# Optimization experiments

Measured on AMD Instinct MI355X. Metric: run time of the kernel, lower is better.

The kernel has to match this reference:

```python
import jax, jax.numpy as jnp
import numpy as np

N = 100000      # nodes (single ntype)
R = 4           # edge types (relations)
E = 160000      # edges per relation
D_IN = 128
D_OUT = 128


def setup_inputs() -> dict:
    key = jax.random.key(0)
    k1, k2, k3, k4, k5 = jax.random.split(key, 5)
    gain = np.sqrt(2.0)  # calculate_gain('relu')
    bound = gain * np.sqrt(6.0 / (D_IN + D_OUT))  # xavier_uniform
    return {
        "x": jax.random.normal(k1, (N, D_IN), dtype=jnp.float32),
        "weight": jax.random.uniform(k2, (R, D_IN, D_OUT), dtype=jnp.float32,
                                     minval=-bound, maxval=bound),
        "loop_weight": jax.random.uniform(k3, (D_IN, D_OUT), dtype=jnp.float32,
                                          minval=-bound, maxval=bound),
        "h_bias": jnp.zeros((D_OUT,), dtype=jnp.float32),
        "src_idx": jax.random.randint(k4, (R, E), 0, N),
        "dst_idx": jax.random.randint(k5, (R, E), 0, N),
    }


def reference(x, weight, loop_weight, h_bias, src_idx, dst_idx):
    # Per-relation GraphConv(norm='right', weight external):
    #   h_r = segment_sum((x @ W_r)[src], dst) / clamp(in_degree, 1)
    # HeteroGraphConv default aggregation sums relations per dst node.
    n = x.shape[0]
    xw = jnp.einsum('nd,rdo->rno', x, weight)  # [R, N, D_OUT]
    h = jnp.zeros((n, weight.shape[2]), dtype=x.dtype)
    ones = jnp.ones((src_idx.shape[1],), dtype=x.dtype)
    for r in range(weight.shape[0]):  # small fixed relation count
        msg = xw[r][src_idx[r]]                                   # [E, D_OUT]
        agg = jax.ops.segment_sum(msg, dst_idx[r], num_segments=n)
        deg = jax.ops.segment_sum(ones, dst_idx[r], num_segments=n)
        h = h + agg / jnp.clip(deg, 1.0)[:, None]                 # norm='right'
    # self-loop + bias + activation (dropout=0 -> identity)
    h = h + x @ loop_weight + h_bias
    return jax.nn.relu(h)
```

## Files before the change

### kernel.cpp

```cpp
#include <hip/hip_runtime.h>

#define DD 128
#define KY 512
#define KT 640
#define RR 4
#define BKT 16
#define CAPS 15
#define NKS (KT / 32)

typedef short short8 __attribute__((ext_vector_type(8)));
typedef float f32x4 __attribute__((ext_vector_type(4)));

union U4S8 { uint4 u; short8 s; };

__device__ __forceinline__ unsigned short f2bf(float f) {
  unsigned u = __float_as_uint(f);
  u += 0x7fffu + ((u >> 16) & 1u);
  return (unsigned short)(u >> 16);
}

__global__ __launch_bounds__(256) void prep(const float* __restrict__ x,
                                            const float* __restrict__ weight,
                                            const float* __restrict__ loopw,
                                            const int* __restrict__ src,
                                            const int* __restrict__ dst,
                                            unsigned short* __restrict__ xb,
                                            unsigned short* __restrict__ wt,
                                            int* __restrict__ slot,
                                            int N, int E, int XB, int WB) {
  int b = blockIdx.x;
  int t = threadIdx.x;
  if (b < XB) {
    int i = b * 256 + t;
    if (i >= (N + 1) * 16) return;
    int n = i >> 4;
    uint4 o = make_uint4(0, 0, 0, 0);
    if (n < N) {
      const float4* xp = (const float4*)x + (size_t)i * 2;
      float4 v0 = xp[0], v1 = xp[1];
      o.x = (unsigned)f2bf(v0.x) | ((unsigned)f2bf(v0.y) << 16);
      o.y = (unsigned)f2bf(v0.z) | ((unsigned)f2bf(v0.w) << 16);
      o.z = (unsigned)f2bf(v1.x) | ((unsigned)f2bf(v1.y) << 16);
      o.w = (unsigned)f2bf(v1.z) | ((unsigned)f2bf(v1.w) << 16);
    }
    ((uint4*)xb)[i] = o;
  } else if (b < XB + WB) {
    int i = (b - XB) * 256 + t;
    if (i >= DD * KT) return;
    int j = i & 7, l = (i >> 3) & 63, c = (i >> 9) & 7, ks = i >> 12;
    int k = ks * 32 + (l >> 4) * 8 + j;
    int col = c * 16 + (l & 15);
    float v = (k < KY) ? weight[(size_t)((k >> 7) * DD + (k & (DD - 1))) * DD + col]
                       : loopw[(size_t)(k - KY) * DD + col];
    wt[i] = f2bf(v);
  } else {
    int i = (b - XB - WB) * 256 + t;
    if (i >= RR * E) return;
    int r = i / E;
    size_t base = ((size_t)dst[i] * RR + r) * BKT;
    int pos = atomicAdd(slot + base, 1);
    if (pos < CAPS) slot[base + 1 + pos] = src[i];
  }
}

__global__ __launch_bounds__(256) void gather_agg(const unsigned* __restrict__ xbu,
                                                  const int* __restrict__ slot,
                                                  unsigned* __restrict__ yu,
                                                  int NN ) {
  int gid = blockIdx.x * 256 + threadIdx.x;
  int n = gid >> 6, lane = gid & 63;
  if (n >= NN) return;
  int N = NN - 1;

  int sv = slot[(size_t)n * 64 + lane];

  int cn[RR], ct[RR];
#pragma unroll
  for (int r = 0; r < RR; r++) {
    ct[r] = __builtin_amdgcn_readlane(sv, r << 4);
    cn[r] = ct[r] > CAPS ? CAPS : ct[r];
  }

  float ax[RR], ay[RR];
#pragma unroll
  for (int r = 0; r < RR; r++) { ax[r] = 0.f; ay[r] = 0.f; }

  int m = max(max(cn[0], cn[1]), max(cn[2], cn[3]));
  for (int i0 = 0; i0 < m; i0 += 4) {
    unsigned vv[4][RR];
#pragma unroll
    for (int u = 0; u < 4; u++) {
#pragma unroll
      for (int r = 0; r < RR; r++) {
        int i = i0 + u;
        int ii = i > 14 ? 14 : i;
        int s = __builtin_amdgcn_readlane(sv, (r << 4) + 1 + ii);
        s = (i < cn[r]) ? s : N;
        vv[u][r] = xbu[(size_t)s * 64 + lane];
      }
    }
#pragma unroll
    for (int u = 0; u < 4; u++)
#pragma unroll
      for (int r = 0; r < RR; r++) {
        ax[r] += __uint_as_float(vv[u][r] << 16);
        ay[r] += __uint_as_float(vv[u][r] & 0xffff0000u);
      }
  }
#pragma unroll
  for (int r = 0; r < RR; r++) {
    float inv = 1.0f / (float)max(ct[r], 1);
    yu[(size_t)n * (KY / 2) + r * 64 + lane] =
        (unsigned)f2bf(ax[r] * inv) | ((unsigned)f2bf(ay[r] * inv) << 16);
  }
}

__global__ __launch_bounds__(512) void gemm_mfma(const unsigned short* __restrict__ y,
                                                 const unsigned short* __restrict__ xb,
                                                 const uint4* __restrict__ wtv,
                                                 const float* __restrict__ bias,
                                                 float* __restrict__ out, int N) {
  __shared__ __align__(16) unsigned short Bs[2][4096];
  int t = threadIdx.x;
  int w = t >> 6, lane = t & 63;
  int m = lane & 15, q = lane >> 4;
  int rb = blockIdx.x * 256;

  int grow0 = rb + w * 32 + m, grow1 = grow0 + 16;
  int r0c = grow0 > N ? N : grow0;
  int r1c = grow1 > N ? N : grow1;
  const unsigned short* ay0 = y  + (size_t)r0c * KY + q * 8;
  const unsigned short* ay1 = y  + (size_t)r1c * KY + q * 8;
  const unsigned short* ax0 = xb + (size_t)r0c * DD + q * 8;
  const unsigned short* ax1 = xb + (size_t)r1c * DD + q * 8;

  *(uint4*)(&Bs[0][t * 8]) = wtv[t];
  __syncthreads();

  f32x4 acc[2][8];
#pragma unroll
  for (int i = 0; i < 2; i++)
#pragma unroll
    for (int c = 0; c < 8; c++) acc[i][c] = (f32x4){0.f, 0.f, 0.f, 0.f};

#pragma unroll
  for (int ks = 0; ks < NKS; ++ks) {
    const int buf = ks & 1;
    uint4 bs;
    if (ks + 1 < NKS) bs = wtv[(size_t)(ks + 1) * 512 + t];

    U4S8 a0, a1;
    if (ks < 16) {
      a0.u = *(const uint4*)(ay0 + ks * 32);
      a1.u = *(const uint4*)(ay1 + ks * 32);
    } else {
      a0.u = *(const uint4*)(ax0 + (ks - 16) * 32);
      a1.u = *(const uint4*)(ax1 + (ks - 16) * 32);
    }

    short8 bb[8];
#pragma unroll
    for (int c = 0; c < 8; ++c)
      bb[c] = *(const short8*)(&Bs[buf][(c * 64 + lane) * 8]);

#pragma unroll
    for (int c = 0; c < 8; ++c) {
      acc[0][c] = __builtin_amdgcn_mfma_f32_16x16x32_bf16(a0.s, bb[c], acc[0][c], 0, 0, 0);
      acc[1][c] = __builtin_amdgcn_mfma_f32_16x16x32_bf16(a1.s, bb[c], acc[1][c], 0, 0, 0);
    }

    if (ks + 1 < NKS) {
      *(uint4*)(&Bs[buf ^ 1][t * 8]) = bs;
      __syncthreads();
    }
  }

  float bv[8];
#pragma unroll
  for (int c = 0; c < 8; ++c) bv[c] = bias[c * 16 + m];
#pragma unroll
  for (int i = 0; i < 2; ++i) {
    int rbase = rb + w * 32 + i * 16 + q * 4;
#pragma unroll
    for (int v = 0; v < 4; ++v) {
      int gr = rbase + v;
      if (gr < N) {
#pragma unroll
        for (int c = 0; c < 8; ++c)
          out[(size_t)gr * DD + c * 16 + m] = fmaxf(acc[i][c][v] + bv[c], 0.f);
      }
    }
  }
}

extern "C" void kernel_launch(void* const* d_in, const int* in_sizes, int n_in,
                              void* d_out, int out_size, void* d_ws, size_t ws_size,
                              hipStream_t stream) {
  const float* x      = (const float*)d_in[0];
  const float* weight = (const float*)d_in[1];
  const float* loop_w = (const float*)d_in[2];
  const float* h_bias = (const float*)d_in[3];
  const int*   src    = (const int*)d_in[4];
  const int*   dst    = (const int*)d_in[5];
  float* out = (float*)d_out;

  const int N = in_sizes[0] / DD;
  const int R = in_sizes[1] / (DD * DD);
  const int E = in_sizes[4] / R;
  const int RE = R * E;

  char* p = (char*)d_ws;
  auto alloc = [&](size_t bytes) {
    char* q = p;
    p += (bytes + 63) & ~size_t(63);
    return q;
  };
  int* slot = (int*)alloc((size_t)(N + 1) * RR * BKT * 4);
  unsigned short* wt = (unsigned short*)alloc((size_t)DD * KT * 2);
  unsigned short* xb = (unsigned short*)alloc((size_t)(N + 1) * DD * 2);
  unsigned short* y  = (unsigned short*)alloc((size_t)(N + 1) * KY * 2);

  hipMemsetAsync(slot, 0, (size_t)(N + 1) * RR * BKT * 4, stream);

  int XB = ((N + 1) * 16 + 255) / 256;
  int WB = (DD * KT + 255) / 256;
  int FB = (RE + 255) / 256;
  prep<<<XB + WB + FB, 256, 0, stream>>>(x, weight, loop_w, src, dst,
                                         xb, wt, slot, N, E, XB, WB);
  gather_agg<<<((size_t)(N + 1) * 64 + 255) / 256, 256, 0, stream>>>(
      (const unsigned*)xb, slot, (unsigned*)y, N + 1);
  gemm_mfma<<<(N + 255) / 256, 512, 0, stream>>>(y, xb, (const uint4*)wt,
                                                 h_bias, out, N);
}
```

Baseline: 230.1 us.

## Fuse neighbor gather-aggregation into the MFMA GEMM via shared-memory A tiles

Merges the gather/mean-aggregation kernel and the bf16 MFMA GEMM into one kernel. Each 256-thread block aggregates 64 nodes' per-relation means into a swizzled LDS tile and then multiplies that tile directly against the weight panels. This removes the intermediate y buffer (N x 512 bf16) write and re-read plus one kernel launch. It also switches the bf16 packing to the hardware v_cvt_pk_bf16_f32 instruction. In exchange it uses about 80KB of LDS per block, which limits occupancy, and each wave now does 16 rows of gather serially before its MFMA work.

```diff
diff --git a/kernel.cpp b/kernel.cpp
--- a/kernel.cpp
+++ b/kernel.cpp
@@ -17,6 +17,12 @@
   unsigned u = __float_as_uint(f);
   u += 0x7fffu + ((u >> 16) & 1u);
   return (unsigned short)(u >> 16);
+}
+
+__device__ __forceinline__ unsigned cvtpk(float lo, float hi) {
+  unsigned r;
+  asm("v_cvt_pk_bf16_f32 %0, %1, %2" : "=v"(r) : "v"(lo), "v"(hi));
+  return r;
 }
 
 __global__ __launch_bounds__(256) void prep(const float* __restrict__ x,
@@ -63,99 +69,112 @@
   }
 }
 
-__global__ __launch_bounds__(256) void gather_agg(const unsigned* __restrict__ xbu,
-                                                  const int* __restrict__ slot,
-                                                  unsigned* __restrict__ yu,
-                                                  int NN ) {
-  int gid = blockIdx.x * 256 + threadIdx.x;
-  int n = gid >> 6, lane = gid & 63;
-  if (n >= NN) return;
-  int N = NN - 1;
-
-  int sv = slot[(size_t)n * 64 + lane];
-
-  int cn[RR], ct[RR];
-#pragma unroll
-  for (int r = 0; r < RR; r++) {
-    ct[r] = __builtin_amdgcn_readlane(sv, r << 4);
-    cn[r] = ct[r] > CAPS ? CAPS : ct[r];
-  }
-
-  float ax[RR], ay[RR];
-#pragma unroll
-  for (int r = 0; r < RR; r++) { ax[r] = 0.f; ay[r] = 0.f; }
-
-  int m = max(max(cn[0], cn[1]), max(cn[2], cn[3]));
-  for (int i0 = 0; i0 < m; i0 += 4) {
-    unsigned vv[4][RR];
-#pragma unroll
-    for (int u = 0; u < 4; u++) {
-#pragma unroll
-      for (int r = 0; r < RR; r++) {
-        int i = i0 + u;
-        int ii = i > 14 ? 14 : i;
-        int s = __builtin_amdgcn_readlane(sv, (r << 4) + 1 + ii);
-        s = (i < cn[r]) ? s : N;
-        vv[u][r] = xbu[(size_t)s * 64 + lane];
-      }
-    }
-#pragma unroll
-    for (int u = 0; u < 4; u++)
-#pragma unroll
-      for (int r = 0; r < RR; r++) {
-        ax[r] += __uint_as_float(vv[u][r] << 16);
-        ay[r] += __uint_as_float(vv[u][r] & 0xffff0000u);
-      }
-  }
-#pragma unroll
-  for (int r = 0; r < RR; r++) {
-    float inv = 1.0f / (float)max(ct[r], 1);
-    yu[(size_t)n * (KY / 2) + r * 64 + lane] =
-        (unsigned)f2bf(ax[r] * inv) | ((unsigned)f2bf(ay[r] * inv) << 16);
-  }
-}
-
-__global__ __launch_bounds__(512) void gemm_mfma(const unsigned short* __restrict__ y,
-                                                 const unsigned short* __restrict__ xb,
-                                                 const uint4* __restrict__ wtv,
-                                                 const float* __restrict__ bias,
-                                                 float* __restrict__ out, int N) {
+__global__ __launch_bounds__(256) void gagemm(const unsigned* __restrict__ xbu,
+                                              const int* __restrict__ slotg,
+                                              const uint4* __restrict__ wtv,
+                                              const float* __restrict__ bias,
+                                              float* __restrict__ out, int N) {
+  __shared__ unsigned As[64 * 256];
   __shared__ __align__(16) unsigned short Bs[2][4096];
   int t = threadIdx.x;
   int w = t >> 6, lane = t & 63;
   int m = lane & 15, q = lane >> 4;
-  int rb = blockIdx.x * 256;
-
-  int grow0 = rb + w * 32 + m, grow1 = grow0 + 16;
-  int r0c = grow0 > N ? N : grow0;
-  int r1c = grow1 > N ? N : grow1;
-  const unsigned short* ay0 = y  + (size_t)r0c * KY + q * 8;
-  const unsigned short* ay1 = y  + (size_t)r1c * KY + q * 8;
-  const unsigned short* ax0 = xb + (size_t)r0c * DD + q * 8;
-  const unsigned short* ax1 = xb + (size_t)r1c * DD + q * 8;
+  int rb = blockIdx.x * 64;
+  int rw = rb + w * 16;
 
   *(uint4*)(&Bs[0][t * 8]) = wtv[t];
+  *(uint4*)(&Bs[0][2048 + t * 8]) = wtv[256 + t];
+
+  int sv[16];
+#pragma unroll
+  for (int j = 0; j < 16; ++j) {
+    int n = rw + j;
+    sv[j] = (n < N) ? slotg[(size_t)n * 64 + lane] : 0;
+  }
+
+#pragma unroll
+  for (int j = 0; j < 16; j += 2) {
+    float ax[2][RR], ay[2][RR];
+    int cn[2][RR];
+    float inv[2][RR];
+#pragma unroll
+    for (int p = 0; p < 2; ++p)
+#pragma unroll
+      for (int r = 0; r < RR; ++r) {
+        int ct = __builtin_amdgcn_readlane(sv[j + p], r << 4);
+        cn[p][r] = ct > CAPS ? CAPS : ct;
+        inv[p][r] = 1.0f / (float)(ct > 1 ? ct : 1);
+        ax[p][r] = 0.f;
+        ay[p][r] = 0.f;
+      }
+    int mm = 0;
+#pragma unroll
+    for (int p = 0; p < 2; ++p)
+#pragma unroll
+      for (int r = 0; r < RR; ++r) mm = max(mm, cn[p][r]);
+
+    for (int i0 = 0; i0 < mm; i0 += 4) {
+      unsigned vv[2][4][RR];
+#pragma unroll
+      for (int u = 0; u < 4; ++u)
+#pragma unroll
+        for (int p = 0; p < 2; ++p)
+#pragma unroll
+          for (int r = 0; r < RR; ++r) {
+            int i = i0 + u;
+            int ii = i > 14 ? 14 : i;
+            int s = __builtin_amdgcn_readlane(sv[j + p], (r << 4) + 1 + ii);
+            s = (i < cn[p][r]) ? s : N;
+            vv[p][u][r] = xbu[(size_t)s * 64 + lane];
+          }
+#pragma unroll
+      for (int p = 0; p < 2; ++p)
+#pragma unroll
+        for (int u = 0; u < 4; ++u)
+#pragma unroll
+          for (int r = 0; r < RR; ++r) {
+            ax[p][r] += __uint_as_float(vv[p][u][r] << 16);
+            ay[p][r] += __uint_as_float(vv[p][u][r] & 0xffff0000u);
+          }
+    }
+#pragma unroll
+    for (int p = 0; p < 2; ++p) {
+      int rr = w * 16 + j + p;
+      int swz = (rr & 7) << 2;
+      unsigned* rowp = As + rr * 256;
+#pragma unroll
+      for (int r = 0; r < RR; ++r)
+        rowp[r * 64 + (lane ^ swz)] =
+            cvtpk(ax[p][r] * inv[p][r], ay[p][r] * inv[p][r]);
+    }
+  }
   __syncthreads();
 
-  f32x4 acc[2][8];
-#pragma unroll
-  for (int i = 0; i < 2; i++)
-#pragma unroll
-    for (int c = 0; c < 8; c++) acc[i][c] = (f32x4){0.f, 0.f, 0.f, 0.f};
+  int rc = rw + m;
+  rc = rc > N ? N : rc;
+  const uint4* axp = (const uint4*)(xbu + (size_t)rc * 64);
+
+  f32x4 acc[8];
+#pragma unroll
+  for (int c = 0; c < 8; ++c) acc[c] = (f32x4){0.f, 0.f, 0.f, 0.f};
+
+  const unsigned* arow = As + (w * 16 + m) * 256;
+  const int aswz = (m & 7) << 2;
 
 #pragma unroll
   for (int ks = 0; ks < NKS; ++ks) {
     const int buf = ks & 1;
-    uint4 bs;
-    if (ks + 1 < NKS) bs = wtv[(size_t)(ks + 1) * 512 + t];
-
-    U4S8 a0, a1;
+    uint4 bs0, bs1;
+    if (ks + 1 < NKS) {
+      bs0 = wtv[(size_t)(ks + 1) * 512 + t];
+      bs1 = wtv[(size_t)(ks + 1) * 512 + 256 + t];
+    }
+
+    U4S8 a;
     if (ks < 16) {
-      a0.u = *(const uint4*)(ay0 + ks * 32);
-      a1.u = *(const uint4*)(ay1 + ks * 32);
+      a.u = *(const uint4*)(arow + ((ks * 16 + q * 4) ^ aswz));
     } else {
-      a0.u = *(const uint4*)(ax0 + (ks - 16) * 32);
-      a1.u = *(const uint4*)(ax1 + (ks - 16) * 32);
+      a.u = axp[(ks - 16) * 4 + q];
     }
 
     short8 bb[8];
@@ -164,13 +183,12 @@
       bb[c] = *(const short8*)(&Bs[buf][(c * 64 + lane) * 8]);
 
 #pragma unroll
-    for (int c = 0; c < 8; ++c) {
-      acc[0][c] = __builtin_amdgcn_mfma_f32_16x16x32_bf16(a0.s, bb[c], acc[0][c], 0, 0, 0);
-      acc[1][c] = __builtin_amdgcn_mfma_f32_16x16x32_bf16(a1.s, bb[c], acc[1][c], 0, 0, 0);
-    }
+    for (int c = 0; c < 8; ++c)
+      acc[c] = __builtin_amdgcn_mfma_f32_16x16x32_bf16(a.s, bb[c], acc[c], 0, 0, 0);
 
     if (ks + 1 < NKS) {
-      *(uint4*)(&Bs[buf ^ 1][t * 8]) = bs;
+      *(uint4*)(&Bs[buf ^ 1][t * 8]) = bs0;
+      *(uint4*)(&Bs[buf ^ 1][2048 + t * 8]) = bs1;
       __syncthreads();
     }
   }
@@ -179,16 +197,12 @@
 #pragma unroll
   for (int c = 0; c < 8; ++c) bv[c] = bias[c * 16 + m];
 #pragma unroll
-  for (int i = 0; i < 2; ++i) {
-    int rbase = rb + w * 32 + i * 16 + q * 4;
-#pragma unroll
-    for (int v = 0; v < 4; ++v) {
-      int gr = rbase + v;
-      if (gr < N) {
-#pragma unroll
-        for (int c = 0; c < 8; ++c)
-          out[(size_t)gr * DD + c * 16 + m] = fmaxf(acc[i][c][v] + bv[c], 0.f);
-      }
+  for (int v = 0; v < 4; ++v) {
+    int gr = rw + q * 4 + v;
+    if (gr < N) {
+#pragma unroll
+      for (int c = 0; c < 8; ++c)
+        out[(size_t)gr * DD + c * 16 + m] = fmaxf(acc[c][v] + bv[c], 0.f);
     }
   }
 }
@@ -218,7 +232,6 @@
   int* slot = (int*)alloc((size_t)(N + 1) * RR * BKT * 4);
   unsigned short* wt = (unsigned short*)alloc((size_t)DD * KT * 2);
   unsigned short* xb = (unsigned short*)alloc((size_t)(N + 1) * DD * 2);
-  unsigned short* y  = (unsigned short*)alloc((size_t)(N + 1) * KY * 2);
 
   hipMemsetAsync(slot, 0, (size_t)(N + 1) * RR * BKT * 4, stream);
 
@@ -227,8 +240,6 @@
   int FB = (RE + 255) / 256;
   prep<<<XB + WB + FB, 256, 0, stream>>>(x, weight, loop_w, src, dst,
                                          xb, wt, slot, N, E, XB, WB);
-  gather_agg<<<((size_t)(N + 1) * 64 + 255) / 256, 256, 0, stream>>>(
-      (const unsigned*)xb, slot, (unsigned*)y, N + 1);
-  gemm_mfma<<<(N + 255) / 256, 512, 0, stream>>>(y, xb, (const uint4*)wt,
-                                                 h_bias, out, N);
-}
+  gagemm<<<(N + 63) / 64, 256, 0, stream>>>((const unsigned*)xb, slot,
+                                            (const uint4*)wt, h_bias, out, N);
+}
```

New measurement: 245.9 us. 1.07x slower.

## Split degree counters from adjacency slots and halve GEMM rows per block

Applied to the files above, without the earlier changes.

Moves the per-(node,relation) in-degree counters out of the slot buckets into a separate deg array, so only that small array has to be zeroed and each bucket holds 16 sources instead of 15. Gather reads the four degrees with one int4 load and uses readfirstlane. The GEMM kernel now covers 128 rows per block with one 16-row MFMA tile per wave instead of two, doubling the block count and halving accumulator registers, but each block loads the weight tiles for half as many rows. Slots left unwritten in a bucket are never read because lookups are masked by degree.

```diff
diff --git a/kernel.cpp b/kernel.cpp
--- a/kernel.cpp
+++ b/kernel.cpp
@@ -4,8 +4,7 @@
 #define KY 512
 #define KT 640
 #define RR 4
-#define BKT 16
-#define CAPS 15
+#define CAP 16
 #define NKS (KT / 32)
 
 typedef short short8 __attribute__((ext_vector_type(8)));
@@ -26,6 +25,7 @@
                                             const int* __restrict__ dst,
                                             unsigned short* __restrict__ xb,
                                             unsigned short* __restrict__ wt,
+                                            int* __restrict__ deg,
                                             int* __restrict__ slot,
                                             int N, int E, int XB, int WB) {
   int b = blockIdx.x;
@@ -57,14 +57,15 @@
     int i = (b - XB - WB) * 256 + t;
     if (i >= RR * E) return;
     int r = i / E;
-    size_t base = ((size_t)dst[i] * RR + r) * BKT;
-    int pos = atomicAdd(slot + base, 1);
-    if (pos < CAPS) slot[base + 1 + pos] = src[i];
+    size_t bk = (size_t)dst[i] * RR + r;
+    int pos = atomicAdd(deg + bk, 1);
+    if (pos < CAP) slot[(bk << 4) + pos] = src[i];
   }
 }
 
 __global__ __launch_bounds__(256) void gather_agg(const unsigned* __restrict__ xbu,
                                                   const int* __restrict__ slot,
+                                                  const int* __restrict__ deg,
                                                   unsigned* __restrict__ yu,
                                                   int NN ) {
   int gid = blockIdx.x * 256 + threadIdx.x;
@@ -73,13 +74,14 @@
   int N = NN - 1;
 
   int sv = slot[(size_t)n * 64 + lane];
-
+  int4 dv = *(const int4*)(deg + (size_t)n * 4);
   int cn[RR], ct[RR];
-#pragma unroll
-  for (int r = 0; r < RR; r++) {
-    ct[r] = __builtin_amdgcn_readlane(sv, r << 4);
-    cn[r] = ct[r] > CAPS ? CAPS : ct[r];
-  }
+  ct[0] = __builtin_amdgcn_readfirstlane(dv.x);
+  ct[1] = __builtin_amdgcn_readfirstlane(dv.y);
+  ct[2] = __builtin_amdgcn_readfirstlane(dv.z);
+  ct[3] = __builtin_amdgcn_readfirstlane(dv.w);
+#pragma unroll
+  for (int r = 0; r < RR; r++) cn[r] = ct[r] > CAP ? CAP : ct[r];
 
   float ax[RR], ay[RR];
 #pragma unroll
@@ -93,8 +95,7 @@
 #pragma unroll
       for (int r = 0; r < RR; r++) {
         int i = i0 + u;
-        int ii = i > 14 ? 14 : i;
-        int s = __builtin_amdgcn_readlane(sv, (r << 4) + 1 + ii);
+        int s = __builtin_amdgcn_readlane(sv, (r << 4) | (i & 15));
         s = (i < cn[r]) ? s : N;
         vv[u][r] = xbu[(size_t)s * 64 + lane];
       }
@@ -124,24 +125,19 @@
   int t = threadIdx.x;
   int w = t >> 6, lane = t & 63;
   int m = lane & 15, q = lane >> 4;
-  int rb = blockIdx.x * 256;
-
-  int grow0 = rb + w * 32 + m, grow1 = grow0 + 16;
-  int r0c = grow0 > N ? N : grow0;
-  int r1c = grow1 > N ? N : grow1;
-  const unsigned short* ay0 = y  + (size_t)r0c * KY + q * 8;
-  const unsigned short* ay1 = y  + (size_t)r1c * KY + q * 8;
-  const unsigned short* ax0 = xb + (size_t)r0c * DD + q * 8;
-  const unsigned short* ax1 = xb + (size_t)r1c * DD + q * 8;
+  int rw = blockIdx.x * 128 + w * 16;
+
+  int rc = rw + m;
+  rc = rc > N ? N : rc;
+  const unsigned short* ay = y  + (size_t)rc * KY + q * 8;
+  const unsigned short* ax = xb + (size_t)rc * DD + q * 8;
 
   *(uint4*)(&Bs[0][t * 8]) = wtv[t];
   __syncthreads();
 
-  f32x4 acc[2][8];
-#pragma unroll
-  for (int i = 0; i < 2; i++)
-#pragma unroll
-    for (int c = 0; c < 8; c++) acc[i][c] = (f32x4){0.f, 0.f, 0.f, 0.f};
+  f32x4 acc[8];
+#pragma unroll
+  for (int c = 0; c < 8; ++c) acc[c] = (f32x4){0.f, 0.f, 0.f, 0.f};
 
 #pragma unroll
   for (int ks = 0; ks < NKS; ++ks) {
@@ -149,14 +145,9 @@
     uint4 bs;
     if (ks + 1 < NKS) bs = wtv[(size_t)(ks + 1) * 512 + t];
 
-    U4S8 a0, a1;
-    if (ks < 16) {
-      a0.u = *(const uint4*)(ay0 + ks * 32);
-      a1.u = *(const uint4*)(ay1 + ks * 32);
-    } else {
-      a0.u = *(const uint4*)(ax0 + (ks - 16) * 32);
-      a1.u = *(const uint4*)(ax1 + (ks - 16) * 32);
-    }
+    U4S8 a;
+    if (ks < 16) a.u = *(const uint4*)(ay + ks * 32);
+    else         a.u = *(const uint4*)(ax + (ks - 16) * 32);
 
     short8 bb[8];
 #pragma unroll
@@ -164,10 +155,8 @@
       bb[c] = *(const short8*)(&Bs[buf][(c * 64 + lane) * 8]);
 
 #pragma unroll
-    for (int c = 0; c < 8; ++c) {
-      acc[0][c] = __builtin_amdgcn_mfma_f32_16x16x32_bf16(a0.s, bb[c], acc[0][c], 0, 0, 0);
-      acc[1][c] = __builtin_amdgcn_mfma_f32_16x16x32_bf16(a1.s, bb[c], acc[1][c], 0, 0, 0);
-    }
+    for (int c = 0; c < 8; ++c)
+      acc[c] = __builtin_amdgcn_mfma_f32_16x16x32_bf16(a.s, bb[c], acc[c], 0, 0, 0);
 
     if (ks + 1 < NKS) {
       *(uint4*)(&Bs[buf ^ 1][t * 8]) = bs;
@@ -179,16 +168,12 @@
 #pragma unroll
   for (int c = 0; c < 8; ++c) bv[c] = bias[c * 16 + m];
 #pragma unroll
-  for (int i = 0; i < 2; ++i) {
-    int rbase = rb + w * 32 + i * 16 + q * 4;
-#pragma unroll
-    for (int v = 0; v < 4; ++v) {
-      int gr = rbase + v;
-      if (gr < N) {
-#pragma unroll
-        for (int c = 0; c < 8; ++c)
-          out[(size_t)gr * DD + c * 16 + m] = fmaxf(acc[i][c][v] + bv[c], 0.f);
-      }
+  for (int v = 0; v < 4; ++v) {
+    int gr = rw + q * 4 + v;
+    if (gr < N) {
+#pragma unroll
+      for (int c = 0; c < 8; ++c)
+        out[(size_t)gr * DD + c * 16 + m] = fmaxf(acc[c][v] + bv[c], 0.f);
     }
   }
 }
@@ -215,20 +200,21 @@
     p += (bytes + 63) & ~size_t(63);
     return q;
   };
-  int* slot = (int*)alloc((size_t)(N + 1) * RR * BKT * 4);
+  int* deg  = (int*)alloc((size_t)(N + 1) * RR * 4);
+  int* slot = (int*)alloc((size_t)(N + 1) * RR * CAP * 4);
   unsigned short* wt = (unsigned short*)alloc((size_t)DD * KT * 2);
   unsigned short* xb = (unsigned short*)alloc((size_t)(N + 1) * DD * 2);
   unsigned short* y  = (unsigned short*)alloc((size_t)(N + 1) * KY * 2);
 
-  hipMemsetAsync(slot, 0, (size_t)(N + 1) * RR * BKT * 4, stream);
+  hipMemsetAsync(deg, 0, (size_t)(N + 1) * RR * 4, stream);
 
   int XB = ((N + 1) * 16 + 255) / 256;
   int WB = (DD * KT + 255) / 256;
   int FB = (RE + 255) / 256;
   prep<<<XB + WB + FB, 256, 0, stream>>>(x, weight, loop_w, src, dst,
-                                         xb, wt, slot, N, E, XB, WB);
+                                         xb, wt, deg, slot, N, E, XB, WB);
   gather_agg<<<((size_t)(N + 1) * 64 + 255) / 256, 256, 0, stream>>>(
-      (const unsigned*)xb, slot, (unsigned*)y, N + 1);
-  gemm_mfma<<<(N + 255) / 256, 512, 0, stream>>>(y, xb, (const uint4*)wt,
+      (const unsigned*)xb, slot, deg, (unsigned*)y, N + 1);
+  gemm_mfma<<<(N + 127) / 128, 512, 0, stream>>>(y, xb, (const uint4*)wt,
                                                  h_bias, out, N);
 }
```

After: 255.3 us. 10.9% more time.
